# Kernel optimization log

Measured on AMD Instinct MI355X. Metric: run time of the kernel, lower is better.

Reference implementation:

```python
import jax, jax.numpy as jnp
import numpy as np

LN_EPS = 1e-5

def setup_inputs() -> dict:
    key = jax.random.key(0)
    k1, k2, k3, k4 = jax.random.split(key, 4)
    B, C_ct, C_b, N = 2, 128, 32, 180
    D = H = W = 24
    ct_feat = jax.random.normal(k1, (B, C_ct, D, H, W), dtype=jnp.float32)
    beam_stack = jax.random.normal(k2, (B, N, C_b, D, H, W), dtype=jnp.float32)
    # 1x1x1 Conv3d query projection == per-voxel linear map C_ct -> C_b
    q_w = jax.random.normal(k3, (C_b, C_ct), dtype=jnp.float32) * (1.0 / np.sqrt(C_ct))
    q_b = jnp.zeros((C_b,), dtype=jnp.float32)
    ln_gamma = jnp.ones((C_b,), dtype=jnp.float32)
    ln_beta = jnp.zeros((C_b,), dtype=jnp.float32)
    return {"ct_feat": ct_feat, "beam_stack": beam_stack, "q_w": q_w,
            "q_b": q_b, "ln_gamma": ln_gamma, "ln_beta": ln_beta}

def reference(ct_feat, beam_stack, q_w, q_b, ln_gamma, ln_beta):
    B, C_ct, D, H, W = ct_feat.shape
    _, N, C_b = beam_stack.shape[:3]
    V = D * H * W
    scale = C_b ** -0.5
    # query: 1x1x1 conv -> [B, V, C_b]
    q = jnp.einsum('oc,bcv->bvo', q_w, ct_feat.reshape(B, C_ct, V)) + q_b
    kv = beam_stack.reshape(B, N, C_b, V)  # [B, N, C_b, V]
    # per-voxel logits over N control points
    logits = jnp.einsum('bvc,bncv->bvn', q, kv) * scale  # [B, V, N]
    attn_w = jax.nn.softmax(logits, axis=-1)
    fused = jnp.einsum('bvn,bncv->bvc', attn_w, kv)  # [B, V, C_b]
    # LayerNorm over channel dim (eps matches torch default)
    mu = jnp.mean(fused, axis=-1, keepdims=True)
    var = jnp.mean(jnp.square(fused - mu), axis=-1, keepdims=True)
    fused = (fused - mu) * jax.lax.rsqrt(var + LN_EPS) * ln_gamma + ln_beta
    fused = fused.transpose(0, 2, 1).reshape(B, C_b, D, H, W)
    return fused, attn_w
```

## Files before the change

kernel.cpp:

```cpp
#include <hip/hip_runtime.h>
#include <math.h>

#define BB      2
#define C_CT    128
#define CB      32
#define NN      180
#define VV      13824
#define VOXB    64
#define GR      4
#define NPG     45
#define THREADS 256

__global__ __launch_bounds__(THREADS, 2)
void vmat_attn_kernel(const float* __restrict__ ct, const float* __restrict__ beam,
                      const float* __restrict__ qw, const float* __restrict__ qb,
                      const float* __restrict__ gam, const float* __restrict__ bet,
                      float* __restrict__ out)
{
    __shared__ __align__(16) float Wbuf[NN * VOXB];
    __shared__ __align__(16) float Pbuf[GR][CB][VOXB];
    __shared__ __align__(16) float l_part[GR][VOXB];
    __shared__ float l_final[VOXB];
    __shared__ float qb_s[CB], gam_s[CB], bet_s[CB];

    const int t    = threadIdx.x;
    const int lane = t & 63;
    const int g    = t >> 6;
    const int vq   = lane & 15;
    const int cg   = lane >> 4;
    const int bid  = blockIdx.x;
    const int b    = bid / (VV / VOXB);
    const int v0   = (bid % (VV / VOXB)) * VOXB;

    for (int i = t; i < CB * C_CT; i += THREADS) Wbuf[i] = qw[i];
    if (t < CB) { qb_s[t] = qb[t]; gam_s[t] = gam[t]; bet_s[t] = bet[t]; }
    __syncthreads();

    {
        const int v = v0 + lane;
        const float* ctp = ct + ((size_t)b * C_CT + g * 32) * VV + v;
        float ctv[32];
        #pragma unroll
        for (int j = 0; j < 32; ++j) ctv[j] = ctp[(size_t)j * VV];
        float qp[CB];
        #pragma unroll
        for (int o = 0; o < CB; ++o) qp[o] = 0.f;
        for (int j = 0; j < 32; ++j) {
            #pragma unroll
            for (int o = 0; o < CB; ++o)
                qp[o] = fmaf(Wbuf[o * C_CT + g * 32 + j], ctv[j], qp[o]);
        }
        #pragma unroll
        for (int o = 0; o < CB; ++o) Pbuf[g][o][lane] = qp[o];
    }
    __syncthreads();

    float q[8][4];
    #pragma unroll
    for (int ci = 0; ci < 8; ++ci) {
        const int o = cg * 8 + ci;
        float4 a0 = *reinterpret_cast<const float4*>(&Pbuf[0][o][vq * 4]);
        float4 a1 = *reinterpret_cast<const float4*>(&Pbuf[1][o][vq * 4]);
        float4 a2 = *reinterpret_cast<const float4*>(&Pbuf[2][o][vq * 4]);
        float4 a3 = *reinterpret_cast<const float4*>(&Pbuf[3][o][vq * 4]);
        q[ci][0] = a0.x + a1.x + a2.x + a3.x + qb_s[o];
        q[ci][1] = a0.y + a1.y + a2.y + a3.y + qb_s[o];
        q[ci][2] = a0.z + a1.z + a2.z + a3.z + qb_s[o];
        q[ci][3] = a0.w + a1.w + a2.w + a3.w + qb_s[o];
    }
    __syncthreads();

    const float scale = 0.17677669529663687f;
    float acc[8][4];
    #pragma unroll
    for (int ci = 0; ci < 8; ++ci)
        acc[ci][0] = acc[ci][1] = acc[ci][2] = acc[ci][3] = 0.f;
    float l0 = 0.f, l1 = 0.f, l2 = 0.f, l3 = 0.f;
    const float* bp0 = beam + (((size_t)b * NN + g * NPG) * CB + cg * 8) * VV + v0 + vq * 4;

    #pragma unroll 1
    for (int i = 0; i < NPG; ++i) {
        const float* bp = bp0 + (size_t)i * CB * VV;
        float4 kv[8];
        #pragma unroll
        for (int ci = 0; ci < 8; ++ci)
            kv[ci] = *reinterpret_cast<const float4*>(bp + (size_t)ci * VV);
        float p0 = 0.f, p1 = 0.f, p2 = 0.f, p3 = 0.f;
        #pragma unroll
        for (int ci = 0; ci < 8; ++ci) {
            p0 = fmaf(q[ci][0], kv[ci].x, p0);
            p1 = fmaf(q[ci][1], kv[ci].y, p1);
            p2 = fmaf(q[ci][2], kv[ci].z, p2);
            p3 = fmaf(q[ci][3], kv[ci].w, p3);
        }
        p0 += __shfl_xor(p0, 16); p1 += __shfl_xor(p1, 16);
        p2 += __shfl_xor(p2, 16); p3 += __shfl_xor(p3, 16);
        p0 += __shfl_xor(p0, 32); p1 += __shfl_xor(p1, 32);
        p2 += __shfl_xor(p2, 32); p3 += __shfl_xor(p3, 32);
        float w0 = __expf(fminf(p0 * scale, 60.f));
        float w1 = __expf(fminf(p1 * scale, 60.f));
        float w2 = __expf(fminf(p2 * scale, 60.f));
        float w3 = __expf(fminf(p3 * scale, 60.f));
        if (cg == 0) {
            float4 wv; wv.x = w0; wv.y = w1; wv.z = w2; wv.w = w3;
            *reinterpret_cast<float4*>(&Wbuf[(g * NPG + i) * VOXB + vq * 4]) = wv;
        }
        l0 += w0; l1 += w1; l2 += w2; l3 += w3;
        #pragma unroll
        for (int ci = 0; ci < 8; ++ci) {
            acc[ci][0] = fmaf(w0, kv[ci].x, acc[ci][0]);
            acc[ci][1] = fmaf(w1, kv[ci].y, acc[ci][1]);
            acc[ci][2] = fmaf(w2, kv[ci].z, acc[ci][2]);
            acc[ci][3] = fmaf(w3, kv[ci].w, acc[ci][3]);
        }
    }

    #pragma unroll
    for (int ci = 0; ci < 8; ++ci) {
        float4 av; av.x = acc[ci][0]; av.y = acc[ci][1]; av.z = acc[ci][2]; av.w = acc[ci][3];
        *reinterpret_cast<float4*>(&Pbuf[g][cg * 8 + ci][vq * 4]) = av;
    }
    if (cg == 0) {
        float4 lv; lv.x = l0; lv.y = l1; lv.z = l2; lv.w = l3;
        *reinterpret_cast<float4*>(&l_part[g][vq * 4]) = lv;
    }
    __syncthreads();

    if (t < VOXB) {
        float lt = l_part[0][t] + l_part[1][t] + l_part[2][t] + l_part[3][t];
        l_final[t] = lt;
        float inv_l = 1.f / lt;
        float f[CB], mu = 0.f;
        #pragma unroll
        for (int c = 0; c < CB; ++c) {
            f[c] = (Pbuf[0][c][t] + Pbuf[1][c][t] + Pbuf[2][c][t] + Pbuf[3][c][t]) * inv_l;
            mu += f[c];
        }
        mu *= (1.f / CB);
        float var = 0.f;
        #pragma unroll
        for (int c = 0; c < CB; ++c) { float d = f[c] - mu; var = fmaf(d, d, var); }
        float rs = rsqrtf(var * (1.f / CB) + 1e-5f);
        float* op = out + (size_t)b * CB * VV + v0 + t;
        #pragma unroll
        for (int c = 0; c < CB; ++c)
            op[(size_t)c * VV] = (f[c] - mu) * rs * gam_s[c] + bet_s[c];
    }
    __syncthreads();

    {
        const int vv = t & 63;
        const int j  = t >> 6;
        const float inv_l = 1.f / l_final[vv];
        float* arow = out + (size_t)BB * CB * VV + ((size_t)b * VV + v0 + vv) * NN;
        const int q4_begin = j * 12;
        const int q4_end   = (j == 3) ? 45 : (j * 12 + 12);
        for (int q4 = q4_begin; q4 < q4_end; ++q4) {
            const int n0 = q4 * 4;
            float4 val;
            val.x = Wbuf[(n0 + 0) * VOXB + vv] * inv_l;
            val.y = Wbuf[(n0 + 1) * VOXB + vv] * inv_l;
            val.z = Wbuf[(n0 + 2) * VOXB + vv] * inv_l;
            val.w = Wbuf[(n0 + 3) * VOXB + vv] * inv_l;
            *reinterpret_cast<float4*>(arow + n0) = val;
        }
    }
}

extern "C" void kernel_launch(void* const* d_in, const int* in_sizes, int n_in,
                              void* d_out, int out_size, void* d_ws, size_t ws_size,
                              hipStream_t stream) {
    (void)in_sizes; (void)n_in; (void)out_size; (void)d_ws; (void)ws_size;
    const float* ct   = (const float*)d_in[0];
    const float* beam = (const float*)d_in[1];
    const float* qw   = (const float*)d_in[2];
    const float* qb   = (const float*)d_in[3];
    const float* gam  = (const float*)d_in[4];
    const float* bet  = (const float*)d_in[5];
    float* out = (float*)d_out;
    dim3 grid(BB * (VV / VOXB));
    vmat_attn_kernel<<<grid, THREADS, 0, stream>>>(ct, beam, qw, qb, gam, bet, out);
}
```

Before: 152.3 us.

## Store attention weights and partial sums in fp16 LDS and double-buffer beam loads

Shared memory is repacked into one aliased 48 KB buffer. The unnormalised softmax weights and the per-group channel accumulators are stored as fp16 instead of fp32, and launch bounds are raised from 2 to 3 blocks per CU to increase occupancy. The beam key/value loads are software-pipelined with two register buffers, so the next control point's loads are issued while the current one is computed. Risks: fp16 rounding or overflow of exp values and accumulators hurts accuracy, and the extra prefetch registers under the tighter launch bound may cause spills.

Result: slower. 214.3 us (+40.7%).

```diff
diff --git a/kernel.cpp b/kernel.cpp
--- a/kernel.cpp
+++ b/kernel.cpp
@@ -1,4 +1,5 @@
 #include <hip/hip_runtime.h>
+#include <hip/hip_fp16.h>
 #include <math.h>
 
 #define BB      2
@@ -11,17 +12,23 @@
 #define NPG     45
 #define THREADS 256
 
-__global__ __launch_bounds__(THREADS, 2)
+#define SMEM_BYTES 49152
+
+__global__ __launch_bounds__(THREADS, 3)
 void vmat_attn_kernel(const float* __restrict__ ct, const float* __restrict__ beam,
                       const float* __restrict__ qw, const float* __restrict__ qb,
                       const float* __restrict__ gam, const float* __restrict__ bet,
                       float* __restrict__ out)
 {
-    __shared__ __align__(16) float Wbuf[NN * VOXB];
-    __shared__ __align__(16) float Pbuf[GR][CB][VOXB];
+    __shared__ __align__(16) unsigned char smem[SMEM_BYTES];
     __shared__ __align__(16) float l_part[GR][VOXB];
     __shared__ float l_final[VOXB];
     __shared__ float qb_s[CB], gam_s[CB], bet_s[CB];
+
+    float*  qw_s  = (float*)smem;
+    float*  qpart = (float*)(smem + 16384);
+    __half* Wbuf  = (__half*)smem;
+    __half* Pacc  = (__half*)(smem + 24576);
 
     const int t    = threadIdx.x;
     const int lane = t & 63;
@@ -32,7 +39,7 @@
     const int b    = bid / (VV / VOXB);
     const int v0   = (bid % (VV / VOXB)) * VOXB;
 
-    for (int i = t; i < CB * C_CT; i += THREADS) Wbuf[i] = qw[i];
+    for (int i = t; i < CB * C_CT; i += THREADS) qw_s[i] = qw[i];
     if (t < CB) { qb_s[t] = qb[t]; gam_s[t] = gam[t]; bet_s[t] = bet[t]; }
     __syncthreads();
 
@@ -48,10 +55,10 @@
         for (int j = 0; j < 32; ++j) {
             #pragma unroll
             for (int o = 0; o < CB; ++o)
-                qp[o] = fmaf(Wbuf[o * C_CT + g * 32 + j], ctv[j], qp[o]);
-        }
-        #pragma unroll
-        for (int o = 0; o < CB; ++o) Pbuf[g][o][lane] = qp[o];
+                qp[o] = fmaf(qw_s[o * C_CT + g * 32 + j], ctv[j], qp[o]);
+        }
+        #pragma unroll
+        for (int o = 0; o < CB; ++o) qpart[(g * CB + o) * VOXB + lane] = qp[o];
     }
     __syncthreads();
 
@@ -59,10 +66,10 @@
     #pragma unroll
     for (int ci = 0; ci < 8; ++ci) {
         const int o = cg * 8 + ci;
-        float4 a0 = *reinterpret_cast<const float4*>(&Pbuf[0][o][vq * 4]);
-        float4 a1 = *reinterpret_cast<const float4*>(&Pbuf[1][o][vq * 4]);
-        float4 a2 = *reinterpret_cast<const float4*>(&Pbuf[2][o][vq * 4]);
-        float4 a3 = *reinterpret_cast<const float4*>(&Pbuf[3][o][vq * 4]);
+        float4 a0 = *reinterpret_cast<const float4*>(&qpart[(0 * CB + o) * VOXB + vq * 4]);
+        float4 a1 = *reinterpret_cast<const float4*>(&qpart[(1 * CB + o) * VOXB + vq * 4]);
+        float4 a2 = *reinterpret_cast<const float4*>(&qpart[(2 * CB + o) * VOXB + vq * 4]);
+        float4 a3 = *reinterpret_cast<const float4*>(&qpart[(3 * CB + o) * VOXB + vq * 4]);
         q[ci][0] = a0.x + a1.x + a2.x + a3.x + qb_s[o];
         q[ci][1] = a0.y + a1.y + a2.y + a3.y + qb_s[o];
         q[ci][2] = a0.z + a1.z + a2.z + a3.z + qb_s[o];
@@ -78,13 +85,14 @@
     float l0 = 0.f, l1 = 0.f, l2 = 0.f, l3 = 0.f;
     const float* bp0 = beam + (((size_t)b * NN + g * NPG) * CB + cg * 8) * VV + v0 + vq * 4;
 
-    #pragma unroll 1
-    for (int i = 0; i < NPG; ++i) {
+    float4 kvA[8], kvB[8];
+    auto loadK = [&](float4* kv, int i) {
         const float* bp = bp0 + (size_t)i * CB * VV;
-        float4 kv[8];
         #pragma unroll
         for (int ci = 0; ci < 8; ++ci)
             kv[ci] = *reinterpret_cast<const float4*>(bp + (size_t)ci * VV);
+    };
+    auto computeK = [&](const float4* kv, int i) {
         float p0 = 0.f, p1 = 0.f, p2 = 0.f, p3 = 0.f;
         #pragma unroll
         for (int ci = 0; ci < 8; ++ci) {
@@ -102,8 +110,9 @@
         float w2 = __expf(fminf(p2 * scale, 60.f));
         float w3 = __expf(fminf(p3 * scale, 60.f));
         if (cg == 0) {
-            float4 wv; wv.x = w0; wv.y = w1; wv.z = w2; wv.w = w3;
-            *reinterpret_cast<float4*>(&Wbuf[(g * NPG + i) * VOXB + vq * 4]) = wv;
+            __half2* wp = reinterpret_cast<__half2*>(&Wbuf[(g * NPG + i) * VOXB + vq * 4]);
+            wp[0] = __floats2half2_rn(w0, w1);
+            wp[1] = __floats2half2_rn(w2, w3);
         }
         l0 += w0; l1 += w1; l2 += w2; l3 += w3;
         #pragma unroll
@@ -113,12 +122,23 @@
             acc[ci][2] = fmaf(w2, kv[ci].z, acc[ci][2]);
             acc[ci][3] = fmaf(w3, kv[ci].w, acc[ci][3]);
         }
-    }
+    };
+
+    loadK(kvA, 0);
+    #pragma unroll 1
+    for (int i = 0; i < NPG - 1; i += 2) {
+        loadK(kvB, i + 1);
+        computeK(kvA, i);
+        if (i + 2 < NPG) loadK(kvA, i + 2);
+        computeK(kvB, i + 1);
+    }
+    computeK(kvA, NPG - 1);
 
     #pragma unroll
     for (int ci = 0; ci < 8; ++ci) {
-        float4 av; av.x = acc[ci][0]; av.y = acc[ci][1]; av.z = acc[ci][2]; av.w = acc[ci][3];
-        *reinterpret_cast<float4*>(&Pbuf[g][cg * 8 + ci][vq * 4]) = av;
+        __half2* ap = reinterpret_cast<__half2*>(&Pacc[((g * CB) + cg * 8 + ci) * VOXB + vq * 4]);
+        ap[0] = __floats2half2_rn(acc[ci][0], acc[ci][1]);
+        ap[1] = __floats2half2_rn(acc[ci][2], acc[ci][3]);
     }
     if (cg == 0) {
         float4 lv; lv.x = l0; lv.y = l1; lv.z = l2; lv.w = l3;
@@ -133,7 +153,10 @@
         float f[CB], mu = 0.f;
         #pragma unroll
         for (int c = 0; c < CB; ++c) {
-            f[c] = (Pbuf[0][c][t] + Pbuf[1][c][t] + Pbuf[2][c][t] + Pbuf[3][c][t]) * inv_l;
+            f[c] = (__half2float(Pacc[(0 * CB + c) * VOXB + t]) +
+                    __half2float(Pacc[(1 * CB + c) * VOXB + t]) +
+                    __half2float(Pacc[(2 * CB + c) * VOXB + t]) +
+                    __half2float(Pacc[(3 * CB + c) * VOXB + t])) * inv_l;
             mu += f[c];
         }
         mu *= (1.f / CB);
@@ -158,10 +181,10 @@
         for (int q4 = q4_begin; q4 < q4_end; ++q4) {
             const int n0 = q4 * 4;
             float4 val;
-            val.x = Wbuf[(n0 + 0) * VOXB + vv] * inv_l;
-            val.y = Wbuf[(n0 + 1) * VOXB + vv] * inv_l;
-            val.z = Wbuf[(n0 + 2) * VOXB + vv] * inv_l;
-            val.w = Wbuf[(n0 + 3) * VOXB + vv] * inv_l;
+            val.x = __half2float(Wbuf[(n0 + 0) * VOXB + vv]) * inv_l;
+            val.y = __half2float(Wbuf[(n0 + 1) * VOXB + vv]) * inv_l;
+            val.z = __half2float(Wbuf[(n0 + 2) * VOXB + vv]) * inv_l;
+            val.w = __half2float(Wbuf[(n0 + 3) * VOXB + vv]) * inv_l;
             *reinterpret_cast<float4*>(arow + n0) = val;
         }
     }
```
